# Kernel optimization log

Measured on AMD Instinct MI355X. Metric: run time of the kernel, lower is better.

Reference implementation:

```python
import jax, jax.numpy as jnp
import numpy as np

T_NO = 501          # refractory kernel length
COS_BASIS_NO = 30   # raised-cosine basis count
SCALE = 7.5
SHIFT = 1


def make_kern_basis():
    # kern_basis[i, t] = 0.5*cos(scale*log(t+shift+1e-7) - pi/2*i) + 0.5, zeroed outside [phi-pi, phi+pi]
    i = np.arange(COS_BASIS_NO, dtype=np.float64)[:, None]
    phi = 0.5 * np.pi * i
    x = np.arange(T_NO, dtype=np.float64)[None, :]
    raw = SCALE * np.log(x + SHIFT + 1e-7)
    basis = 0.5 * np.cos(raw - phi) + 0.5
    basis = np.where((raw < phi - np.pi) | (raw > phi + np.pi), 0.0, basis)
    return jnp.asarray(basis, jnp.float32)  # [30, T_NO]


def setup_inputs() -> dict:
    key = jax.random.key(0)
    ks = jax.random.split(key, 7)
    B, T = 64, 2048
    H_no = 5
    return {
        "V": jax.random.normal(ks[0], (B, T), jnp.float32),
        "D": jax.random.normal(ks[1], (B, T), jnp.float32),
        "w1": jax.random.normal(ks[2], (H_no, 2, 1), jnp.float32) * 0.5,   # Conv1d(2->H, k=1)
        "b1": jax.random.normal(ks[3], (H_no,), jnp.float32) * 0.1,
        "w2": jax.random.normal(ks[4], (1, H_no, 1), jnp.float32) * 0.5,   # Conv1d(H->1, k=1)
        "b2": jax.random.normal(ks[5], (1,), jnp.float32) * 0.1,
        "W_refract": jax.random.normal(ks[6], (COS_BASIS_NO,), jnp.float32) * 0.01,
    }


def reference(V, D, w1, b1, w2, b2, W_refract):
    B, T = V.shape
    kern_basis = make_kern_basis()
    refract_kern = jnp.flip(kern_basis.T @ W_refract)  # [T_NO], flipped as in torch

    # Ring-buffer alignment: sample at time s lives in column s % T_NO. At time t,
    # the original weights the window [t-T_NO, t-1] with refract_kern[0..T_NO-1]
    # (oldest -> kern[0]), i.e. column c gets weight refract_kern[(c - t) % T_NO].
    idx = (jnp.arange(T_NO)[None, :] - jnp.arange(T_NO)[:, None]) % T_NO
    kern_table = refract_kern[idx]  # [T_NO, T_NO]; kern_table[t % T_NO] is weights for step t

    # K_no=1, L_no=2 -> pointwise MLP: tanh(Conv1x1(2->H)) then Conv1x1(H->1)
    x = jnp.stack([V, D], axis=1)                                        # [B, 2, T]
    h = jnp.tanh(jnp.einsum('hc,bct->bht', w1[:, :, 0], x) + b1[None, :, None])
    nn_out = jnp.einsum('h,bht->bt', w2[0, :, 0], h) + b2[0]             # [B, T]

    key0 = jax.random.key(42)

    def step(carry, xs):
        ring, key = carry
        t, nn_t = xs                                   # nn_t: [B]
        key, sub = jax.random.split(key)
        p = t % T_NO
        refract = ring @ kern_table[p]                 # [B] sliding-window sum
        P_t = jax.nn.sigmoid(nn_t + refract)
        spike = jax.random.bernoulli(sub, P_t).astype(V.dtype)
        ring = ring.at[:, p].set(spike)                # overwrite slot that just expired
        return (ring, key), (spike, P_t)

    ring0 = jnp.zeros((B, T_NO), V.dtype)
    (_, _), (S_seq, P_seq) = jax.lax.scan(step, (ring0, key0), (jnp.arange(T), nn_out.T))
    S_out = S_seq.T  # [B, T]
    P_out = P_seq.T  # [B, T]
    return S_out, P_out
```

## Files before the change

kernel.cpp:

```cpp
#include <hip/hip_runtime.h>
#include <stdint.h>

typedef unsigned long long ull;

#define TT 2048

struct TF2 { uint32_t x, y; };

constexpr TF2 tf2x32(uint32_t k0, uint32_t k1, uint32_t x0, uint32_t x1) {
  uint32_t ks2 = k0 ^ k1 ^ 0x1BD11BDAu;
  x0 += k0; x1 += k1;
#define TFR_(r) x0 += x1; x1 = __builtin_rotateleft32(x1, r); x1 ^= x0;
  TFR_(13) TFR_(15) TFR_(26) TFR_(6)
  x0 += k1;  x1 += ks2 + 1u;
  TFR_(17) TFR_(29) TFR_(16) TFR_(24)
  x0 += ks2; x1 += k0 + 2u;
  TFR_(13) TFR_(15) TFR_(26) TFR_(6)
  x0 += k0;  x1 += k1 + 3u;
  TFR_(17) TFR_(29) TFR_(16) TFR_(24)
  x0 += k1;  x1 += ks2 + 4u;
  TFR_(13) TFR_(15) TFR_(26) TFR_(6)
  x0 += ks2; x1 += k0 + 5u;
#undef TFR_
  return {x0, x1};
}

struct Half_ { uint32_t a[1024]; uint32_t b[1024]; uint32_t k0, k1; };

constexpr Half_ make_half(uint32_t k0, uint32_t k1) {
  Half_ h{};
  for (int t = 0; t < 1024; ++t) {
    TF2 nk = tf2x32(k0, k1, 0u, 0u);
    TF2 sb = tf2x32(k0, k1, 0u, 1u);
    h.a[t] = sb.x; h.b[t] = sb.y;
    k0 = nk.x; k1 = nk.y;
  }
  h.k0 = k0; h.k1 = k1;
  return h;
}

namespace ckeys {
constexpr Half_ H0 = make_half(0u, 42u);
constexpr Half_ H1 = make_half(H0.k0, H0.k1);
}
__constant__ Half_ dH0 = ckeys::H0;
__constant__ Half_ dH1 = ckeys::H1;

__device__ __forceinline__ float tanh_xla(float x) {
#pragma clang fp contract(off)
  float ax = fabsf(x);
  float xc = fminf(fmaxf(x, -7.90531110763549805f), 7.90531110763549805f);
  float x2 = xc * xc;
  float p = fmaf(x2, -2.76076847742355e-16f, 2.00018790482477e-13f);
  p = fmaf(x2, p, -8.60467152213735e-11f);
  p = fmaf(x2, p, 5.12229709037114e-08f);
  p = fmaf(x2, p, 1.48572235717979e-05f);
  p = fmaf(x2, p, 6.37261928875436e-04f);
  p = fmaf(x2, p, 4.89352455891786e-03f);
  p = xc * p;
  float q = fmaf(x2, 1.19825839466702e-06f, 1.18534705686654e-04f);
  q = fmaf(x2, q, 2.26843463243900e-03f);
  q = fmaf(x2, q, 4.89352518554385e-03f);
  return (ax < 0.0004f) ? x : (p / q);
}

__device__ __forceinline__ float sig_ref(float z) {
#pragma clang fp contract(off)
  float e = (float)exp(-(double)z);
  return 1.0f / (1.0f + e);
}

__device__ __forceinline__ uint32_t ford(float f) {
  uint32_t x = __float_as_uint(f);
  return (x & 0x80000000u) ? ~x : (x | 0x80000000u);
}
__device__ __forceinline__ float fdec(uint32_t k) {
  uint32_t b = (k & 0x80000000u) ? (k & 0x7fffffffu) : ~k;
  return __uint_as_float(b);
}

__device__ float find_tau(float u) {
  if (!(u > 0.0f)) return -1.0e30f;
  double zg = log((double)u / (1.0 - (double)u));
  float zgf = (float)zg;
  zgf = fminf(fmaxf(zgf, -90.0f), 90.0f);
  uint32_t kc = ford(zgf);
  uint32_t klo = kc - 96u, khi = kc + 96u;
  if (!(sig_ref(fdec(klo)) <= u)) klo = ford(-95.0f);
  if (!(sig_ref(fdec(khi)) > u))  khi = ford(95.0f);
  while (khi - klo > 1u) {
    uint32_t km = klo + ((khi - klo) >> 1);
    if (sig_ref(fdec(km)) <= u) klo = km; else khi = km;
  }
  return fdec(klo);
}

__global__ void ap_pre_kernel(const float* __restrict__ V, const float* __restrict__ D,
                              const float* __restrict__ w1, const float* __restrict__ b1,
                              const float* __restrict__ w2, const float* __restrict__ b2,
                              const float* __restrict__ Wr,
                              float* __restrict__ zb, float* __restrict__ tauA,
                              float* __restrict__ rk, uint32_t* flags) {
#pragma clang fp contract(off)
  int tid = threadIdx.x;
  int blk = blockIdx.x;
  if (blk < 512) {
    int idx = blk * 256 + tid;
    int b = idx >> 11, t = idx & 2047;
    float v = V[idx], dd = D[idx];
    float acc = 0.f;
#pragma unroll
    for (int h = 0; h < 5; ++h) {
      float m = fmaf(w1[2 * h + 1], dd, w1[2 * h] * v) + b1[h];
      float th = tanh_xla(m);
      acc = (h == 0) ? (w2[0] * th) : fmaf(w2[h], th, acc);
    }
    float z0 = acc + b2[0];
    uint32_t ka = (t < 1024) ? dH0.a[t] : dH1.a[t - 1024];
    uint32_t kb = (t < 1024) ? dH0.b[t] : dH1.b[t - 1024];
    TF2 o = tf2x32(ka, kb, 0u, (uint32_t)b);
    uint32_t bits = o.x ^ o.y;
    float u = __uint_as_float((bits >> 9) | 0x3f800000u) - 1.0f;
    zb[t * 64 + b] = z0;
    tauA[t * 64 + b] = find_tau(u);
  } else if (blk < 514) {
    int d = (blk - 512) * 256 + tid;
    float val = 0.f;
    if (d >= 1 && d <= 501) {
      double raw = 7.5 * log((double)(d - 1) + 1.0 + 1e-7);
      float a = 0.f;
      for (int i = 0; i < 30; ++i) {
        double phi = (0.5 * 3.141592653589793) * (double)i;
        float bf;
        if (raw < phi - 3.141592653589793 || raw > phi + 3.141592653589793) bf = 0.f;
        else bf = (float)(0.5 * cos(raw - phi) + 0.5);
        a = fmaf(Wr[i], bf, a);
      }
      val = a;
    }
    rk[d] = val;
  } else {
    if (tid == 0) flags[0] = 0u;
    if (tid >= 1 && tid <= 64) {
      int c = tid - 1;
      flags[tid] = (c <= 4) ? 4u : 0u;
    }
  }
}

__global__ void __launch_bounds__(512, 1)
ap_main_kernel(float* zb, const float* __restrict__ tauA,
               const float* __restrict__ rk, float* __restrict__ zarr,
               ull* __restrict__ sw, uint32_t* flags) {
  __shared__ float lutS[6 * 256];
  __shared__ float lutM[14 * 256];
  __shared__ float4 comboQ[64 * 64];
  __shared__ uint32_t snapR[16 * 64];
  __shared__ int winDoneA[8];
  __shared__ int winDoneB[8];
  __shared__ int progLds;
  __shared__ ull swL[384];
  __shared__ uint32_t colb[64 * 13];
  __shared__ float rkL[512];

  int tid = threadIdx.x;
  int lane = tid & 63;

  if (blockIdx.x == 0) {
    for (int e = tid; e < 6 * 256; e += 512) {
      int o = e >> 8, vb = e & 255;
      float s = 0.f;
      for (int i = 0; i < 8; ++i)
        if (vb & (1 << i)) s += rk[3 + 8 * o + i];
      lutS[e] = s;
    }
    for (int e = tid; e < 14 * 256; e += 512) {
      int o = 6 + (e >> 8), vb = e & 255;
      float s = 0.f;
      if (o <= 9) {
        for (int i = 0; i < 8; ++i)
          if ((vb >> (7 - i)) & 1) s += rk[3 + 8 * o + i];
      } else {
        for (int i = 0; i < 8; ++i)
          if ((vb >> i) & 1) s += rk[3 + 8 * o + 7 - i];
      }
      lutM[e] = s;
    }
    if (tid < 8) { winDoneA[tid] = 0; winDoneB[tid] = 0; }
    if (tid == 0) progLds = 0;
    __syncthreads();

    int wv = tid >> 6;

    if (wv == 0) {
      float rk1 = rk[1], rk2 = rk[2];
      auto pollWin = [&](int vv) {
        int slot = vv & 7, gen = vv + 1;
        while (__hip_atomic_load(&winDoneA[slot], __ATOMIC_ACQUIRE, __HIP_MEMORY_SCOPE_WORKGROUP) != gen ||
               __hip_atomic_load(&winDoneB[slot], __ATOMIC_ACQUIRE, __HIP_MEMORY_SCOPE_WORKGROUP) != gen)
          __builtin_amdgcn_s_sleep(1);
      };
      pollWin(0); pollWin(1);
      float4 cp4[2];
      cp4[0] = comboQ[0 * 64 + lane];
      cp4[1] = comboQ[1 * 64 + lane];
      float l[2][6];
#pragma unroll
      for (int k = 0; k < 6; ++k) { l[0][k] = 0.f; l[1][k] = 0.f; }
      uint32_t m0 = 0, m1 = 0;
      float s1f = 0.f, s2f = 0.f;

      for (int w = 0; w < 128; ++w) {
        if (w + 1 < 128) pollWin(w + 1);
        int baseLo = ((16 * w + 2) & 63) * 64 + lane;
        int baseHi = ((16 * w + 16) & 63) * 64 + lane;
        float* zarrW = zarr + w * 1024 + lane;
#pragma unroll
        for (int q = 0; q < 16; ++q) {
          int p = q & 1;
          float4 f4 = cp4[p];
          float a1 = l[p][0] + l[p][1];
          float a2 = l[p][2] + l[p][3];
          float A  = a1 + a2;
          float b1 = l[p][4] + l[p][5];
          float B  = b1 + f4.y;
          float g  = (A + B) + f4.z;
          float z  = f4.x + g;
          z = fmaf(rk2, s2f, z);
          z = fmaf(rk1, s1f, z);
          bool sp = z > f4.w;
          zarrW[q * 64] = z;
          cp4[p] = (q < 14) ? comboQ[baseLo + q * 64] : comboQ[baseHi + (q - 14) * 64];
          l[p][0] = lutS[         (m0        & 255u)];
          l[p][1] = lutS[ 256 + ((m0 >> 8 ) & 255u)];
          l[p][2] = lutS[ 512 + ((m0 >> 16) & 255u)];
          l[p][3] = lutS[ 768 + ( m0 >> 24         )];
          l[p][4] = lutS[1024 + ( m1        & 255u)];
          l[p][5] = lutS[1280 + ((m1 >> 8 ) & 255u)];
          m1 = __builtin_amdgcn_alignbit(m1, m0, 31);
          m0 = (m0 << 1) | (sp ? 1u : 0u);
          s2f = s1f;
          s1f = sp ? 1.0f : 0.0f;
        }
        snapR[(w & 15) * 64 + lane] = m0;
        if (lane == 0)
          __hip_atomic_store(&progLds, 16 * w + 16, __ATOMIC_RELEASE,
                             __HIP_MEMORY_SCOPE_WORKGROUP);
      }
      return;
    } else if (wv >= 1 && wv <= 4) {
      int cConf = 4;
      for (int v = wv - 1; v < 128; v += 4) {
        if (v >= 4) {
          int tgt = 16 * v - 48;
          while (__hip_atomic_load(&progLds, __ATOMIC_ACQUIRE,
                                   __HIP_MEMORY_SCOPE_WORKGROUP) < tgt)
            __builtin_amdgcn_s_sleep(1);
        }
        int c = v >> 1;
        if (c >= 5 && c > cConf) {
          while (__hip_atomic_load(&flags[1 + c], __ATOMIC_ACQUIRE,
                                   __HIP_MEMORY_SCOPE_AGENT) < 4u)
            __builtin_amdgcn_s_sleep(2);
          cConf = c;
        }
        uint32_t a[8];
#pragma unroll
        for (int j = 0; j < 8; ++j) {
          int g = v - 11 + j;
          a[j] = (g >= 0) ? __builtin_bitreverse32(snapR[(g & 15) * 64 + lane]) : 0u;
        }
        uint32_t r[4];
        r[0] = (a[0] >> 16) | (a[1] & 0xFFFF0000u);
        r[1] = (a[2] >> 16) | (a[3] & 0xFFFF0000u);
        r[2] = (a[4] >> 16) | (a[5] & 0xFFFF0000u);
        r[3] = (a[6] >> 16) | (a[7] & 0xFFFF0000u);
        const float* zvp = zb + 16 * v * 64 + lane;
        const float* tvp = tauA + 16 * v * 64 + lane;
        float zv[16], tv[16];
#pragma unroll
        for (int q = 0; q < 16; ++q) { zv[q] = zvp[q * 64]; tv[q] = tvp[q * 64]; }
#pragma unroll
        for (int q = 0; q < 16; ++q) {
          float e8 = 0.f, e9 = 0.f, acc = 0.f;
#pragma unroll
          for (int o = 8; o < 20; ++o) {
            int pos = q + 166 - 8 * o;
            int k = pos >> 5, sh = pos & 31;
            uint32_t byt;
            if (sh <= 24) byt = (r[k] >> sh) & 255u;
            else          byt = __builtin_amdgcn_alignbit(r[k + 1], r[k], (uint32_t)sh) & 255u;
            float ent = lutM[(o - 6) * 256 + byt];
            if (o == 8) e8 = ent;
            else if (o == 9) e9 = ent;
            else acc += ent;
          }
          float P89 = e8 + e9;
          float combo = zv[q] + acc;
          int idx = ((16 * v + q) & 63) * 64 + lane;
          comboQ[idx].x = combo;
          *(float2*)((float*)&comboQ[idx] + 2) = make_float2(P89, tv[q]);
        }
        if (lane == 0)
          __hip_atomic_store(&winDoneA[v & 7], v + 1, __ATOMIC_RELEASE,
                             __HIP_MEMORY_SCOPE_WORKGROUP);
      }
      return;
    } else if (wv == 5 || wv == 6) {
      for (int v = wv - 5; v < 128; v += 2) {
        if (v >= 3) {
          int tgt = 16 * v - 32;
          while (__hip_atomic_load(&progLds, __ATOMIC_ACQUIRE,
                                   __HIP_MEMORY_SCOPE_WORKGROUP) < tgt)
            __builtin_amdgcn_s_sleep(1);
        }
        uint32_t a2[4];
#pragma unroll
        for (int j = 0; j < 4; ++j) {
          int g = v - 6 + j;
          a2[j] = (g >= 0) ? __builtin_bitreverse32(snapR[(g & 15) * 64 + lane]) : 0u;
        }
        uint32_t r2[2];
        r2[0] = (a2[0] >> 16) | (a2[1] & 0xFFFF0000u);
        r2[1] = (a2[2] >> 16) | (a2[3] & 0xFFFF0000u);
#pragma unroll
        for (int q = 0; q < 16; ++q) {
          float e6, e7;
          {
            int pos = q + 38;
            int sh = pos & 31;
            uint32_t byt = (r2[1] >> sh) & 255u;
            e6 = lutM[0 * 256 + byt];
          }
          {
            int pos = q + 30;
            int k = pos >> 5, sh = pos & 31;
            uint32_t byt;
            if (sh <= 24) byt = (r2[k] >> sh) & 255u;
            else          byt = __builtin_amdgcn_alignbit(r2[k + 1], r2[k], (uint32_t)sh) & 255u;
            e7 = lutM[1 * 256 + byt];
          }
          float P67 = e6 + e7;
          int idx = ((16 * v + q) & 63) * 64 + lane;
          ((float*)&comboQ[idx])[1] = P67;
        }
        if (lane == 0)
          __hip_atomic_store(&winDoneB[v & 7], v + 1, __ATOMIC_RELEASE,
                             __HIP_MEMORY_SCOPE_WORKGROUP);
      }
      return;
    } else {
      for (int m = 1; m <= 64; ++m) {
        while (__hip_atomic_load(&progLds, __ATOMIC_ACQUIRE,
                                 __HIP_MEMORY_SCOPE_WORKGROUP) < 32 * m)
          __builtin_amdgcn_s_sleep(2);
        uint32_t sA = snapR[((2 * m - 2) & 15) * 64 + lane];
        uint32_t sB = snapR[((2 * m - 1) & 15) * 64 + lane];
#pragma unroll
        for (int i = 0; i < 32; ++i) {
          uint32_t sn = (i < 16) ? sA : sB;
          uint32_t bit = (sn >> (15 - (i & 15))) & 1u;
          ull bal = __ballot(bit != 0u);
          if (lane == 0) sw[32 * (m - 1) + i] = bal;
        }
        if (lane == 0)
          __hip_atomic_store(&flags[0], (uint32_t)m, __ATOMIC_RELEASE,
                             __HIP_MEMORY_SCOPE_AGENT);
      }
      return;
    }
  }

  int c = 5 + ((int)blockIdx.x - 1) / 4;
  int qq = ((int)blockIdx.x - 1) & 3;
  int T0 = 32 * c + 8 * qq;
  int s0 = T0 - 501;
  if (tid == 0) {
    while ((int)__hip_atomic_load(&flags[0], __ATOMIC_ACQUIRE,
                                  __HIP_MEMORY_SCOPE_AGENT) < c - 4)
      __builtin_amdgcn_s_sleep(8);
  }
  __syncthreads();
  for (int i = tid; i < 384; i += 512) {
    int s = s0 + i;
    swL[i] = (s >= 0 && i < 346) ? sw[s] : 0ull;
  }
  rkL[tid] = rk[tid];
  __syncthreads();
  {
    int w8 = tid >> 6;
#pragma unroll
    for (int rep = 0; rep < 2; ++rep) {
      int W = w8 + 8 * rep;
      if (W < 12) {
        uint32_t word = 0;
        for (int i2 = 0; i2 < 32; ++i2) {
          ull v = swL[32 * W + i2];
          uint32_t bit = (uint32_t)((v >> lane) & 1ull);
          word |= bit << i2;
        }
        colb[lane * 13 + W] = word;
      }
    }
  }
  __syncthreads();
  {
    int tl = tid >> 6;
    int b = tid & 63;
    uint32_t cw[12];
#pragma unroll
    for (int W = 0; W < 12; ++W) cw[W] = colb[b * 13 + W];
    uint32_t A[11];
#pragma unroll
    for (int W = 0; W < 11; ++W)
      A[W] = __builtin_amdgcn_alignbit(cw[W + 1], cw[W], (uint32_t)tl);
    float acc = 0.f;
#pragma unroll 4
    for (int k = 0; k < 339; ++k) {
      float bv = (float)((A[k >> 5] >> (k & 31)) & 1u);
      acc = fmaf(bv, rkL[501 - k], acc);
    }
    int t = T0 + tl;
    zb[t * 64 + b] += acc;
  }
  __syncthreads();
  if (tid == 0)
    __hip_atomic_fetch_add(&flags[1 + c], 1u, __ATOMIC_RELEASE,
                           __HIP_MEMORY_SCOPE_AGENT);
}

__global__ void ap_post_kernel(const float* __restrict__ zarr, const float* __restrict__ tauA,
                               float* __restrict__ out) {
#pragma clang fp contract(off)
  int idx = blockIdx.x * 256 + threadIdx.x;
  int b = idx >> 11, t = idx & 2047;
  float z = zarr[t * 64 + b];
  float tau = tauA[t * 64 + b];
  out[idx] = (z > tau) ? 1.0f : 0.0f;
  out[131072 + idx] = 1.0f / (1.0f + __expf(-z));
}

extern "C" void kernel_launch(void* const* d_in, const int* in_sizes, int n_in,
                              void* d_out, int out_size, void* d_ws, size_t ws_size,
                              hipStream_t stream) {
  (void)in_sizes; (void)n_in; (void)out_size; (void)ws_size;
  const float* V  = (const float*)d_in[0];
  const float* D  = (const float*)d_in[1];
  const float* w1 = (const float*)d_in[2];
  const float* b1 = (const float*)d_in[3];
  const float* w2 = (const float*)d_in[4];
  const float* b2 = (const float*)d_in[5];
  const float* Wr = (const float*)d_in[6];

  char* w = (char*)d_ws;
  float*    zb    = (float*)w;
  float*    tauA  = (float*)(w + 0x080000);
  float*    zarr  = (float*)(w + 0x100000);
  ull*      swp   = (ull*)(w + 0x180000);
  float*    rk    = (float*)(w + 0x184000);
  uint32_t* flags = (uint32_t*)(w + 0x184800);

  ap_pre_kernel<<<515, 256, 0, stream>>>(V, D, w1, b1, w2, b2, Wr, zb, tauA, rk, flags);
  ap_main_kernel<<<237, 512, 0, stream>>>(zb, tauA, rk, zarr, swp, flags);
  ap_post_kernel<<<512, 256, 0, stream>>>(zarr, tauA, (float*)d_out);
}
```

Before: 507.0 us.

## Widen serial recurrence window to 32 steps with 8-byte local LUT

The serial spike-recurrence wave now processes 32-step windows instead of 16, and its local lookup table grows from 6 to 8 byte-chunks, so the near-window history it sums directly extends further back. The producer waves are reorganised so that four helper waves each compute 8 of the 32 steps per window, and the separate helper waves for the middle chunks are dropped. The ballot wave now emits one snapshot per window. The goal is to halve per-window sync and polling overhead on the critical serial wave and balance producer work, at the cost of two extra LDS lookups per step in the serial loop and a deeper producer lead requirement.

```diff
diff --git a/kernel.cpp b/kernel.cpp
--- a/kernel.cpp
+++ b/kernel.cpp
@@ -140,11 +140,8 @@
     }
     rk[d] = val;
   } else {
-    if (tid == 0) flags[0] = 0u;
-    if (tid >= 1 && tid <= 64) {
-      int c = tid - 1;
-      flags[tid] = (c <= 4) ? 4u : 0u;
-    }
+    if (tid < 80) flags[tid] = 0u;
+    if (tid >= 1 && tid <= 5) flags[tid] = 4u;
   }
 }
 
@@ -152,12 +149,11 @@
 ap_main_kernel(float* zb, const float* __restrict__ tauA,
                const float* __restrict__ rk, float* __restrict__ zarr,
                ull* __restrict__ sw, uint32_t* flags) {
-  __shared__ float lutS[6 * 256];
-  __shared__ float lutM[14 * 256];
+  __shared__ float lutS[8 * 256];
+  __shared__ float lutM[12 * 256];
   __shared__ float4 comboQ[64 * 64];
   __shared__ uint32_t snapR[16 * 64];
-  __shared__ int winDoneA[8];
-  __shared__ int winDoneB[8];
+  __shared__ int winDoneH[4][8];
   __shared__ int progLds;
   __shared__ ull swL[384];
   __shared__ uint32_t colb[64 * 13];
@@ -167,26 +163,21 @@
   int lane = tid & 63;
 
   if (blockIdx.x == 0) {
-    for (int e = tid; e < 6 * 256; e += 512) {
+    for (int e = tid; e < 8 * 256; e += 512) {
       int o = e >> 8, vb = e & 255;
       float s = 0.f;
       for (int i = 0; i < 8; ++i)
         if (vb & (1 << i)) s += rk[3 + 8 * o + i];
       lutS[e] = s;
     }
-    for (int e = tid; e < 14 * 256; e += 512) {
-      int o = 6 + (e >> 8), vb = e & 255;
+    for (int e = tid; e < 12 * 256; e += 512) {
+      int o = 8 + (e >> 8), vb = e & 255;
       float s = 0.f;
-      if (o <= 9) {
-        for (int i = 0; i < 8; ++i)
-          if ((vb >> (7 - i)) & 1) s += rk[3 + 8 * o + i];
-      } else {
-        for (int i = 0; i < 8; ++i)
-          if ((vb >> i) & 1) s += rk[3 + 8 * o + 7 - i];
-      }
+      for (int i = 0; i < 8; ++i)
+        if ((vb >> i) & 1) s += rk[10 + 8 * o - i];
       lutM[e] = s;
     }
-    if (tid < 8) { winDoneA[tid] = 0; winDoneB[tid] = 0; }
+    if (tid < 32) winDoneH[tid >> 3][tid & 7] = 0;
     if (tid == 0) progLds = 0;
     __syncthreads();
 
@@ -196,47 +187,53 @@
       float rk1 = rk[1], rk2 = rk[2];
       auto pollWin = [&](int vv) {
         int slot = vv & 7, gen = vv + 1;
-        while (__hip_atomic_load(&winDoneA[slot], __ATOMIC_ACQUIRE, __HIP_MEMORY_SCOPE_WORKGROUP) != gen ||
-               __hip_atomic_load(&winDoneB[slot], __ATOMIC_ACQUIRE, __HIP_MEMORY_SCOPE_WORKGROUP) != gen)
+        for (;;) {
+          int ok = 1;
+#pragma unroll
+          for (int h = 0; h < 4; ++h)
+            ok &= (__hip_atomic_load(&winDoneH[h][slot], __ATOMIC_ACQUIRE,
+                                     __HIP_MEMORY_SCOPE_WORKGROUP) == gen);
+          if (ok) break;
           __builtin_amdgcn_s_sleep(1);
+        }
       };
-      pollWin(0); pollWin(1);
+      pollWin(0);
       float4 cp4[2];
       cp4[0] = comboQ[0 * 64 + lane];
       cp4[1] = comboQ[1 * 64 + lane];
-      float l[2][6];
-#pragma unroll
-      for (int k = 0; k < 6; ++k) { l[0][k] = 0.f; l[1][k] = 0.f; }
+      float l[2][8];
+#pragma unroll
+      for (int k = 0; k < 8; ++k) { l[0][k] = 0.f; l[1][k] = 0.f; }
       uint32_t m0 = 0, m1 = 0;
       float s1f = 0.f, s2f = 0.f;
 
-      for (int w = 0; w < 128; ++w) {
-        if (w + 1 < 128) pollWin(w + 1);
-        int baseLo = ((16 * w + 2) & 63) * 64 + lane;
-        int baseHi = ((16 * w + 16) & 63) * 64 + lane;
-        float* zarrW = zarr + w * 1024 + lane;
-#pragma unroll
-        for (int q = 0; q < 16; ++q) {
+      for (int w = 0; w < 64; ++w) {
+        float* zarrW = zarr + w * 2048 + lane;
+#pragma unroll
+        for (int q = 0; q < 32; ++q) {
+          if (q == 30 && w + 1 < 64) pollWin(w + 1);
           int p = q & 1;
           float4 f4 = cp4[p];
           float a1 = l[p][0] + l[p][1];
           float a2 = l[p][2] + l[p][3];
           float A  = a1 + a2;
-          float b1 = l[p][4] + l[p][5];
-          float B  = b1 + f4.y;
-          float g  = (A + B) + f4.z;
+          float b1_ = l[p][4] + l[p][5];
+          float B  = b1_ + (l[p][6] + l[p][7]);
+          float g  = (A + B) + f4.y;
           float z  = f4.x + g;
           z = fmaf(rk2, s2f, z);
           z = fmaf(rk1, s1f, z);
-          bool sp = z > f4.w;
+          bool sp = z > f4.z;
           zarrW[q * 64] = z;
-          cp4[p] = (q < 14) ? comboQ[baseLo + q * 64] : comboQ[baseHi + (q - 14) * 64];
+          cp4[p] = comboQ[(((32 * w + q + 2) & 63) << 6) + lane];
           l[p][0] = lutS[         (m0        & 255u)];
           l[p][1] = lutS[ 256 + ((m0 >> 8 ) & 255u)];
           l[p][2] = lutS[ 512 + ((m0 >> 16) & 255u)];
           l[p][3] = lutS[ 768 + ( m0 >> 24         )];
           l[p][4] = lutS[1024 + ( m1        & 255u)];
           l[p][5] = lutS[1280 + ((m1 >> 8 ) & 255u)];
+          l[p][6] = lutS[1536 + ((m1 >> 16) & 255u)];
+          l[p][7] = lutS[1792 + ( m1 >> 24         )];
           m1 = __builtin_amdgcn_alignbit(m1, m0, 31);
           m0 = (m0 << 1) | (sp ? 1u : 0u);
           s2f = s1f;
@@ -244,131 +241,82 @@
         }
         snapR[(w & 15) * 64 + lane] = m0;
         if (lane == 0)
-          __hip_atomic_store(&progLds, 16 * w + 16, __ATOMIC_RELEASE,
+          __hip_atomic_store(&progLds, 32 * w + 32, __ATOMIC_RELEASE,
                              __HIP_MEMORY_SCOPE_WORKGROUP);
       }
       return;
     } else if (wv >= 1 && wv <= 4) {
-      int cConf = 4;
-      for (int v = wv - 1; v < 128; v += 4) {
-        if (v >= 4) {
-          int tgt = 16 * v - 48;
+      int h = wv - 1;
+      int q0 = 8 * h;
+      for (int v = 0; v < 64; ++v) {
+        if (v >= 2) {
+          int tgt = 32 * (v - 1);
           while (__hip_atomic_load(&progLds, __ATOMIC_ACQUIRE,
                                    __HIP_MEMORY_SCOPE_WORKGROUP) < tgt)
             __builtin_amdgcn_s_sleep(1);
         }
-        int c = v >> 1;
-        if (c >= 5 && c > cConf) {
-          while (__hip_atomic_load(&flags[1 + c], __ATOMIC_ACQUIRE,
+        if (v >= 5) {
+          while (__hip_atomic_load(&flags[1 + v], __ATOMIC_ACQUIRE,
                                    __HIP_MEMORY_SCOPE_AGENT) < 4u)
             __builtin_amdgcn_s_sleep(2);
-          cConf = c;
-        }
-        uint32_t a[8];
-#pragma unroll
-        for (int j = 0; j < 8; ++j) {
-          int g = v - 11 + j;
-          a[j] = (g >= 0) ? __builtin_bitreverse32(snapR[(g & 15) * 64 + lane]) : 0u;
-        }
-        uint32_t r[4];
-        r[0] = (a[0] >> 16) | (a[1] & 0xFFFF0000u);
-        r[1] = (a[2] >> 16) | (a[3] & 0xFFFF0000u);
-        r[2] = (a[4] >> 16) | (a[5] & 0xFFFF0000u);
-        r[3] = (a[6] >> 16) | (a[7] & 0xFFFF0000u);
-        const float* zvp = zb + 16 * v * 64 + lane;
-        const float* tvp = tauA + 16 * v * 64 + lane;
-        float zv[16], tv[16];
-#pragma unroll
-        for (int q = 0; q < 16; ++q) { zv[q] = zvp[q * 64]; tv[q] = tvp[q * 64]; }
-#pragma unroll
-        for (int q = 0; q < 16; ++q) {
+        }
+        uint32_t r[5];
+#pragma unroll
+        for (int j = 0; j < 5; ++j) {
+          int g = v - 6 + j;
+          r[j] = (g >= 0) ? __builtin_bitreverse32(snapR[(g & 15) * 64 + lane]) : 0u;
+        }
+        const float* zvp = zb   + (32 * v + q0) * 64 + lane;
+        const float* tvp = tauA + (32 * v + q0) * 64 + lane;
+        float zv[8], tv[8];
+#pragma unroll
+        for (int qq = 0; qq < 8; ++qq) { zv[qq] = zvp[qq * 64]; tv[qq] = tvp[qq * 64]; }
+#pragma unroll
+        for (int qq = 0; qq < 8; ++qq) {
+          int q = q0 + qq;
           float e8 = 0.f, e9 = 0.f, acc = 0.f;
 #pragma unroll
           for (int o = 8; o < 20; ++o) {
-            int pos = q + 166 - 8 * o;
+            int pos = q + 182 - 8 * o;
             int k = pos >> 5, sh = pos & 31;
             uint32_t byt;
             if (sh <= 24) byt = (r[k] >> sh) & 255u;
             else          byt = __builtin_amdgcn_alignbit(r[k + 1], r[k], (uint32_t)sh) & 255u;
-            float ent = lutM[(o - 6) * 256 + byt];
+            float ent = lutM[(o - 8) * 256 + byt];
             if (o == 8) e8 = ent;
             else if (o == 9) e9 = ent;
             else acc += ent;
           }
-          float P89 = e8 + e9;
-          float combo = zv[q] + acc;
-          int idx = ((16 * v + q) & 63) * 64 + lane;
-          comboQ[idx].x = combo;
-          *(float2*)((float*)&comboQ[idx] + 2) = make_float2(P89, tv[q]);
-        }
-        if (lane == 0)
-          __hip_atomic_store(&winDoneA[v & 7], v + 1, __ATOMIC_RELEASE,
-                             __HIP_MEMORY_SCOPE_WORKGROUP);
+          float4 f4;
+          f4.x = zv[qq] + acc;
+          f4.y = e8 + e9;
+          f4.z = tv[qq];
+          f4.w = 0.f;
+          comboQ[(((32 * v + q) & 63) << 6) + lane] = f4;
+        }
+        __hip_atomic_store(&winDoneH[h][v & 7], v + 1, __ATOMIC_RELEASE,
+                           __HIP_MEMORY_SCOPE_WORKGROUP);
       }
       return;
-    } else if (wv == 5 || wv == 6) {
-      for (int v = wv - 5; v < 128; v += 2) {
-        if (v >= 3) {
-          int tgt = 16 * v - 32;
-          while (__hip_atomic_load(&progLds, __ATOMIC_ACQUIRE,
-                                   __HIP_MEMORY_SCOPE_WORKGROUP) < tgt)
-            __builtin_amdgcn_s_sleep(1);
-        }
-        uint32_t a2[4];
-#pragma unroll
-        for (int j = 0; j < 4; ++j) {
-          int g = v - 6 + j;
-          a2[j] = (g >= 0) ? __builtin_bitreverse32(snapR[(g & 15) * 64 + lane]) : 0u;
-        }
-        uint32_t r2[2];
-        r2[0] = (a2[0] >> 16) | (a2[1] & 0xFFFF0000u);
-        r2[1] = (a2[2] >> 16) | (a2[3] & 0xFFFF0000u);
-#pragma unroll
-        for (int q = 0; q < 16; ++q) {
-          float e6, e7;
-          {
-            int pos = q + 38;
-            int sh = pos & 31;
-            uint32_t byt = (r2[1] >> sh) & 255u;
-            e6 = lutM[0 * 256 + byt];
-          }
-          {
-            int pos = q + 30;
-            int k = pos >> 5, sh = pos & 31;
-            uint32_t byt;
-            if (sh <= 24) byt = (r2[k] >> sh) & 255u;
-            else          byt = __builtin_amdgcn_alignbit(r2[k + 1], r2[k], (uint32_t)sh) & 255u;
-            e7 = lutM[1 * 256 + byt];
-          }
-          float P67 = e6 + e7;
-          int idx = ((16 * v + q) & 63) * 64 + lane;
-          ((float*)&comboQ[idx])[1] = P67;
+    } else if (wv == 5) {
+      for (int u = 0; u < 64; ++u) {
+        while (__hip_atomic_load(&progLds, __ATOMIC_ACQUIRE,
+                                 __HIP_MEMORY_SCOPE_WORKGROUP) < 32 * u + 32)
+          __builtin_amdgcn_s_sleep(2);
+        uint32_t sn = snapR[(u & 15) * 64 + lane];
+#pragma unroll
+        for (int i = 0; i < 32; ++i) {
+          uint32_t bit = (sn >> (31 - i)) & 1u;
+          ull bal = __ballot(bit != 0u);
+          if (lane == 0) sw[32 * u + i] = bal;
         }
         if (lane == 0)
-          __hip_atomic_store(&winDoneB[v & 7], v + 1, __ATOMIC_RELEASE,
-                             __HIP_MEMORY_SCOPE_WORKGROUP);
-      }
-      return;
-    } else {
-      for (int m = 1; m <= 64; ++m) {
-        while (__hip_atomic_load(&progLds, __ATOMIC_ACQUIRE,
-                                 __HIP_MEMORY_SCOPE_WORKGROUP) < 32 * m)
-          __builtin_amdgcn_s_sleep(2);
-        uint32_t sA = snapR[((2 * m - 2) & 15) * 64 + lane];
-        uint32_t sB = snapR[((2 * m - 1) & 15) * 64 + lane];
-#pragma unroll
-        for (int i = 0; i < 32; ++i) {
-          uint32_t sn = (i < 16) ? sA : sB;
-          uint32_t bit = (sn >> (15 - (i & 15))) & 1u;
-          ull bal = __ballot(bit != 0u);
-          if (lane == 0) sw[32 * (m - 1) + i] = bal;
-        }
-        if (lane == 0)
-          __hip_atomic_store(&flags[0], (uint32_t)m, __ATOMIC_RELEASE,
+          __hip_atomic_store(&flags[0], (uint32_t)(u + 1), __ATOMIC_RELEASE,
                              __HIP_MEMORY_SCOPE_AGENT);
       }
       return;
     }
+    return;
   }
 
   int c = 5 + ((int)blockIdx.x - 1) / 4;
```

Measured after the change: 1.090 ms. 2.15x slower.
